# Kernel tuning notes

Hardware: AMD Instinct MI355X
Metric: run time of the kernel (lower is better)

## Reference

```python
import jax, jax.numpy as jnp
import numpy as np

N = 100000   # nodes
E = 1000000  # edges
DIN = 128    # atom_in_features
DE = 16      # edge_attr_dim
H = 128      # hidden width (preprocess/cheb/postprocess)
K = 3        # Chebyshev order
EPS = 1e-5


def setup_inputs() -> dict:
    key = jax.random.key(0)
    ks = jax.random.split(key, 16)
    s = 0.02
    return {
        "x": jax.random.normal(ks[0], (N, DIN), jnp.float32),
        "edge_index": jax.random.randint(ks[1], (2, E), 0, N),
        "edge_attr": jax.random.normal(ks[2], (E, DE), jnp.float32),
        # AtomEdgeInteraction linear: (DIN+DE) -> H
        "w_int": jax.random.normal(ks[3], (DIN + DE, H), jnp.float32) * s,
        "b_int": jnp.zeros((H,), jnp.float32),
        # preprocess layer 1: Linear + BatchNorm + ReLU
        "w_pre": jax.random.normal(ks[4], (H, H), jnp.float32) * s,
        "b_pre": jnp.zeros((H,), jnp.float32),
        "g_pre": jnp.ones((H,), jnp.float32),
        "be_pre": jnp.zeros((H,), jnp.float32),
        # ChebConv layers: weight [K, in, out] + bias
        "cheb1_w": jax.random.normal(ks[5], (K, H, H), jnp.float32) * s,
        "cheb1_b": jnp.zeros((H,), jnp.float32),
        "cheb2_w": jax.random.normal(ks[6], (K, H, H), jnp.float32) * s,
        "cheb2_b": jnp.zeros((H,), jnp.float32),
        # postprocess: Linear + BatchNorm + ReLU
        "w_post": jax.random.normal(ks[7], (H, H), jnp.float32) * s,
        "b_post": jnp.zeros((H,), jnp.float32),
        "g_post": jnp.ones((H,), jnp.float32),
        "be_post": jnp.zeros((H,), jnp.float32),
        # output layer H -> 1
        "w_out": jax.random.normal(ks[8], (H, 1), jnp.float32) * s,
        "b_out": jnp.zeros((1,), jnp.float32),
    }


def _bn(z, g, b):
    # BatchNorm1d, training-mode batch statistics (biased variance, like torch)
    m = z.mean(0)
    v = ((z - m) ** 2).mean(0)
    return g * (z - m) * jax.lax.rsqrt(v + EPS) + b


def _cheb(h, W, b, row, col, norm):
    # ChebConv with sym normalization, lambda_max=2 => L_hat = -D^{-1/2} A D^{-1/2}
    def lhat(z):
        return jax.ops.segment_sum(norm[:, None] * z[row], col, num_segments=N)

    Tx0 = h
    out = Tx0 @ W[0]
    Tx1 = lhat(Tx0)
    out = out + Tx1 @ W[1]
    for k in range(2, W.shape[0]):
        Tx2 = 2.0 * lhat(Tx1) - Tx0
        out = out + Tx2 @ W[k]
        Tx0, Tx1 = Tx1, Tx2
    return out + b


def reference(x, edge_index, edge_attr,
              w_int, b_int,
              w_pre, b_pre, g_pre, be_pre,
              cheb1_w, cheb1_b, cheb2_w, cheb2_b,
              w_post, b_post, g_post, be_post,
              w_out, b_out):
    row, col = edge_index[0], edge_index[1]
    ones_e = jnp.ones((E,), x.dtype)

    # AtomEdgeInteraction: gather -> concat -> linear -> scatter_mean over col
    comb = jnp.concatenate([x[row], edge_attr], axis=-1)  # [E, DIN+DE]
    upd = comb @ w_int + b_int                             # [E, H]
    cnt = jax.ops.segment_sum(ones_e, col, num_segments=N)
    h = jax.ops.segment_sum(upd, col, num_segments=N) / jnp.clip(cnt, 1.0)[:, None]

    # preprocess layer 1 (Linear + BN + ReLU; dropout rate 0)
    h = jax.nn.relu(_bn(h @ w_pre + b_pre, g_pre, be_pre))

    # sym-normalized edge coefficients for scaled Laplacian
    deg = jax.ops.segment_sum(ones_e, row, num_segments=N)
    dis = jnp.where(deg > 0, jax.lax.rsqrt(jnp.maximum(deg, 1.0)), 0.0)
    norm = -dis[row] * dis[col]  # [E]

    h = jax.nn.relu(_cheb(h, cheb1_w, cheb1_b, row, col, norm))
    h = jax.nn.relu(_cheb(h, cheb2_w, cheb2_b, row, col, norm))

    # postprocess (Linear + BN + ReLU)
    h = jax.nn.relu(_bn(h @ w_post + b_post, g_post, be_post))

    # output layer, squeeze(-1) -> [N]
    return (h @ w_out + b_out).squeeze(-1)
```

## Files before the change

### kernel.cpp

```cpp
#include <hip/hip_runtime.h>
#include <hip/hip_bf16.h>

using u16 = unsigned short;
using u32 = unsigned int;

#define NN 100000
#define NE 1000000

typedef __attribute__((ext_vector_type(8))) short bfrag;
typedef __attribute__((ext_vector_type(4))) float ffrag;

#define BF16ONE2 0x3F803F80u

__device__ __forceinline__ float bf2f(u16 u) { return __uint_as_float(((u32)u) << 16); }
__device__ __forceinline__ u16 f2bf(float f) {
  u32 x = __float_as_uint(f);
  return (u16)((x + 0x7fffu + ((x >> 16) & 1u)) >> 16);
}
__device__ __forceinline__ float rdv(const void* p, long i, int f) {
  return f ? bf2f(((const u16*)p)[i]) : ((const float*)p)[i];
}
__device__ __forceinline__ void acc8(float* a, uint4 v, float w) {
  a[0] = fmaf(w, __uint_as_float(v.x << 16), a[0]);
  a[1] = fmaf(w, __uint_as_float(v.x & 0xffff0000u), a[1]);
  a[2] = fmaf(w, __uint_as_float(v.y << 16), a[2]);
  a[3] = fmaf(w, __uint_as_float(v.y & 0xffff0000u), a[3]);
  a[4] = fmaf(w, __uint_as_float(v.z << 16), a[4]);
  a[5] = fmaf(w, __uint_as_float(v.z & 0xffff0000u), a[5]);
  a[6] = fmaf(w, __uint_as_float(v.w << 16), a[6]);
  a[7] = fmaf(w, __uint_as_float(v.w & 0xffff0000u), a[7]);
}

#define OWXT 0
#define OWPRE 16384
#define OWD1 32768
#define OW11 49152
#define OV21 65536
#define OWD2 81920
#define OW12 98304
#define OV22 114688
#define OWPOST 131072
#define OWET 147456

#define ASTRIDE 136
#define ESTRIDE 132

struct PrepArgs { const void* in[16]; };

__global__ void k_prep(PrepArgs a, const u32* __restrict__ gp, u16* __restrict__ wq,
                       float* __restrict__ wf) {
  int t = blockIdx.x * 256 + threadIdx.x;
  int f = (gp[0] == BF16ONE2) ? 1 : 0;
  if (t < 16384) {
    int o = t >> 7, k = t & 127;
    int ko = k * 128 + o;
    int ok = o * 128 + k;
    wq[OWXT + ok] = f2bf(rdv(a.in[0], ko, f));
    wq[OWPRE + ok] = f2bf(rdv(a.in[2], ko, f));
    float c0 = rdv(a.in[6], ko, f);
    float c1 = rdv(a.in[6], 16384 + ko, f);
    float c2 = rdv(a.in[6], 32768 + ko, f);
    wq[OWD1 + ok] = f2bf(c0 - c2);
    wq[OW11 + ok] = f2bf(c1);
    wq[OV21 + ok] = f2bf(2.f * c2);
    float d0 = rdv(a.in[8], ko, f);
    float d1 = rdv(a.in[8], 16384 + ko, f);
    float d2 = rdv(a.in[8], 32768 + ko, f);
    wq[OWD2 + ok] = f2bf(d0 - d2);
    wq[OW12 + ok] = f2bf(d1);
    wq[OV22 + ok] = f2bf(2.f * d2);
    wq[OWPOST + ok] = f2bf(rdv(a.in[10], ko, f));
  }
  if (t < 4096) {
    int o = t >> 5, k = t & 31;
    wq[OWET + o * 32 + k] = (k < 16) ? f2bf(rdv(a.in[0], (long)(128 + k) * 128 + o, f)) : (u16)0;
  }
  if (t < 1281) {
    int s = t >> 7, j = t & 127;
    const int map[11] = {1, 3, 4, 5, 7, 9, 11, 12, 13, 14, 15};
    wf[t] = rdv(a.in[map[s]], j, f);
  }
}

__global__ void k_hist(const int* __restrict__ ei, int* cnt) {
  long t = (long)blockIdx.x * 256 + threadIdx.x;
  long e0 = t * 8;
  if (e0 + 8 <= NE) {
    int4 c0 = *(const int4*)(ei + NE + e0);
    int4 c1 = *(const int4*)(ei + NE + e0 + 4);
    atomicAdd(&cnt[c0.x], 1);
    atomicAdd(&cnt[c0.y], 1);
    atomicAdd(&cnt[c0.z], 1);
    atomicAdd(&cnt[c0.w], 1);
    atomicAdd(&cnt[c1.x], 1);
    atomicAdd(&cnt[c1.y], 1);
    atomicAdd(&cnt[c1.z], 1);
    atomicAdd(&cnt[c1.w], 1);
  } else {
    for (long e = e0; e < NE; e++) atomicAdd(&cnt[ei[NE + e]], 1);
  }
}

__global__ void k_scan1(const int* __restrict__ cnt, int* off, int* bsum) {
  __shared__ int s[1024];
  int t = threadIdx.x;
  int g = blockIdx.x * 1024 + t;
  int v = (g < NN) ? cnt[g] : 0;
  s[t] = v;
  __syncthreads();
  for (int st = 1; st < 1024; st <<= 1) {
    int x = (t >= st) ? s[t - st] : 0;
    __syncthreads();
    s[t] += x;
    __syncthreads();
  }
  if (g < NN) off[g] = s[t] - v;
  if (t == 1023) bsum[blockIdx.x] = s[t];
}

__global__ void k_scan23(int* off, const int* __restrict__ bsum, int* cur, int nb) {
  __shared__ int s[128];
  int t = threadIdx.x;
  int v = 0;
  if (t < 128) {
    v = (t < nb) ? bsum[t] : 0;
    s[t] = v;
  }
  __syncthreads();
  for (int st = 1; st < 128; st <<= 1) {
    int x = (t >= st && t < 128) ? s[t - st] : 0;
    __syncthreads();
    if (t < 128) s[t] += x;
    __syncthreads();
  }
  if (t < 128) s[t] -= v;
  __syncthreads();
  int pre = s[blockIdx.x];
  int g = blockIdx.x * 1024 + t;
  if (g < NN) {
    int o = off[g] + pre;
    off[g] = o;
    cur[g] = o;
  }
  if (g == 0) off[NN] = NE;
}

__global__ void k_place(const int* __restrict__ ei, int* cur, int* deg,
                        int* __restrict__ crow, int* __restrict__ ceid) {
  long t = (long)blockIdx.x * 256 + threadIdx.x;
  long e0 = t * 8;
  if (e0 + 8 <= NE) {
    int4 r0 = *(const int4*)(ei + e0);
    int4 r1 = *(const int4*)(ei + e0 + 4);
    int4 c0 = *(const int4*)(ei + NE + e0);
    int4 c1 = *(const int4*)(ei + NE + e0 + 4);
    int r[8] = {r0.x, r0.y, r0.z, r0.w, r1.x, r1.y, r1.z, r1.w};
    int c[8] = {c0.x, c0.y, c0.z, c0.w, c1.x, c1.y, c1.z, c1.w};
    int p[8];
#pragma unroll
    for (int i = 0; i < 8; i++) p[i] = atomicAdd(&cur[c[i]], 1);
#pragma unroll
    for (int i = 0; i < 8; i++) atomicAdd(&deg[r[i]], 1);
#pragma unroll
    for (int i = 0; i < 8; i++) crow[p[i]] = r[i];
#pragma unroll
    for (int i = 0; i < 8; i++) ceid[p[i]] = (int)(e0 + i);
  } else {
    for (long e = e0; e < NE; e++) {
      int rr = ei[e], cc = ei[NE + e];
      int p = atomicAdd(&cur[cc], 1);
      atomicAdd(&deg[rr], 1);
      crow[p] = rr;
      ceid[p] = (int)e;
    }
  }
}

__global__ void k_dis(const int* __restrict__ deg, float* __restrict__ dis) {
  int g = blockIdx.x * 256 + threadIdx.x;
  if (g >= NN) return;
  int d = deg[g];
  dis[g] = d > 0 ? rsqrtf((float)d) : 0.f;
}

__global__ __launch_bounds__(256) void k_spmm(const u16* __restrict__ src,
                                              u16* __restrict__ dst,
                                              const int* __restrict__ off,
                                              const int* __restrict__ crow,
                                              const float* __restrict__ cnorm) {
  int t = threadIdx.x;
  int node = blockIdx.x * 8 + (t >> 5);
  if (node >= NN) return;
  int l = t & 31;
  int half = l >> 4;
  int c = (l & 15) * 8;
  int p0 = off[node], p1 = off[node + 1];
  float a[8];
#pragma unroll
  for (int j = 0; j < 8; j++) a[j] = 0.f;
  const u16* sp = src + c;
  int p = p0 + half;
  for (; p + 6 < p1; p += 8) {
    int r0 = crow[p], r1 = crow[p + 2], r2 = crow[p + 4], r3 = crow[p + 6];
    float w0 = cnorm[p], w1 = cnorm[p + 2], w2 = cnorm[p + 4], w3 = cnorm[p + 6];
    uint4 v0 = *(const uint4*)(sp + (long)r0 * 128);
    uint4 v1 = *(const uint4*)(sp + (long)r1 * 128);
    uint4 v2 = *(const uint4*)(sp + (long)r2 * 128);
    uint4 v3 = *(const uint4*)(sp + (long)r3 * 128);
    acc8(a, v0, w0);
    acc8(a, v1, w1);
    acc8(a, v2, w2);
    acc8(a, v3, w3);
  }
  for (; p < p1; p += 2) acc8(a, *(const uint4*)(sp + (long)crow[p] * 128), cnorm[p]);
#pragma unroll
  for (int j = 0; j < 8; j++) a[j] += __shfl_xor(a[j], 16);
  if (half) return;
  uint4 o;
  o.x = (u32)f2bf(a[0]) | ((u32)f2bf(a[1]) << 16);
  o.y = (u32)f2bf(a[2]) | ((u32)f2bf(a[3]) << 16);
  o.z = (u32)f2bf(a[4]) | ((u32)f2bf(a[5]) << 16);
  o.w = (u32)f2bf(a[6]) | ((u32)f2bf(a[7]) << 16);
  *(uint4*)(dst + (long)node * 128 + c) = o;
}

template <int WEIGHTED>
__device__ __forceinline__ void gather_lds(u16* sA, const u16* __restrict__ src,
                                           const int* __restrict__ off,
                                           const int* __restrict__ crow,
                                           const float* __restrict__ cnorm, int r0) {
  int tid = threadIdx.x;
  int grp = tid >> 4;
  int c = (tid & 15) * 8;
  const u16* sp = src + c;
#pragma unroll
  for (int i = 0; i < 4; i++) {
    int nl = grp * 4 + i;
    int node = r0 + nl;
    float a[8];
#pragma unroll
    for (int j = 0; j < 8; j++) a[j] = 0.f;
    if (node < NN) {
      int p0 = off[node], p1 = off[node + 1];
      int p = p0;
      for (; p + 4 <= p1; p += 4) {
        int r0i = crow[p], r1i = crow[p + 1], r2i = crow[p + 2], r3i = crow[p + 3];
        float w0 = WEIGHTED ? cnorm[p] : 1.f;
        float w1 = WEIGHTED ? cnorm[p + 1] : 1.f;
        float w2 = WEIGHTED ? cnorm[p + 2] : 1.f;
        float w3 = WEIGHTED ? cnorm[p + 3] : 1.f;
        uint4 v0 = *(const uint4*)(sp + (long)r0i * 128);
        uint4 v1 = *(const uint4*)(sp + (long)r1i * 128);
        uint4 v2 = *(const uint4*)(sp + (long)r2i * 128);
        uint4 v3 = *(const uint4*)(sp + (long)r3i * 128);
        acc8(a, v0, w0);
        acc8(a, v1, w1);
        acc8(a, v2, w2);
        acc8(a, v3, w3);
      }
      for (; p < p1; p++)
        acc8(a, *(const uint4*)(sp + (long)crow[p] * 128), WEIGHTED ? cnorm[p] : 1.f);
    }
    uint4 o;
    o.x = (u32)f2bf(a[0]) | ((u32)f2bf(a[1]) << 16);
    o.y = (u32)f2bf(a[2]) | ((u32)f2bf(a[3]) << 16);
    o.z = (u32)f2bf(a[4]) | ((u32)f2bf(a[5]) << 16);
    o.w = (u32)f2bf(a[6]) | ((u32)f2bf(a[7]) << 16);
    *(uint4*)(sA + nl * ASTRIDE + c) = o;
  }
}

__global__ __launch_bounds__(256) void k_asum(const void* __restrict__ eattr,
                                              const u32* __restrict__ gp,
                                              u16* __restrict__ asum,
                                              const int* __restrict__ off,
                                              const int* __restrict__ ceid,
                                              const int* __restrict__ crow,
                                              const float* __restrict__ dis,
                                              float* __restrict__ cnorm) {
  int t = blockIdx.x * 256 + threadIdx.x;
  int node = t >> 4;
  if (node >= NN) return;
  int j = t & 15;
  int p0 = off[node], p1 = off[node + 1];
  float ndis = -dis[node];
  for (int p = p0 + j; p < p1; p += 16) cnorm[p] = ndis * dis[crow[p]];
  float a = 0.f;
  if (gp[0] == BF16ONE2) {
    const u16* e16 = (const u16*)eattr;
    int p = p0;
    for (; p + 4 <= p1; p += 4) {
      float v0 = bf2f(e16[(long)ceid[p] * 16 + j]);
      float v1 = bf2f(e16[(long)ceid[p + 1] * 16 + j]);
      float v2 = bf2f(e16[(long)ceid[p + 2] * 16 + j]);
      float v3 = bf2f(e16[(long)ceid[p + 3] * 16 + j]);
      a += v0 + v1 + v2 + v3;
    }
    for (; p < p1; p++) a += bf2f(e16[(long)ceid[p] * 16 + j]);
  } else {
    const float* e32 = (const float*)eattr;
    int p = p0;
    for (; p + 4 <= p1; p += 4) {
      float v0 = e32[(long)ceid[p] * 16 + j];
      float v1 = e32[(long)ceid[p + 1] * 16 + j];
      float v2 = e32[(long)ceid[p + 2] * 16 + j];
      float v3 = e32[(long)ceid[p + 3] * 16 + j];
      a += v0 + v1 + v2 + v3;
    }
    for (; p < p1; p++) a += e32[(long)ceid[p] * 16 + j];
  }
  asum[(long)node * 16 + j] = f2bf(a);
}

struct MArgs {
  const void* A0; const u16* W0T; int a0raw;
  const float* bias;
  u16* out;
  const u32* gp;
  float* part;
};

__global__ __launch_bounds__(256) void k_mgemm(MArgs m) {
  constexpr int ROWS = 128, RT = 8, TPR = 2, SEGW = 64;
  __shared__ __align__(16) u16 sA[ROWS * ASTRIDE];
  int tid = threadIdx.x;
  int wv = tid >> 6, lane = tid & 63;
  int col16 = lane & 15, quad = lane >> 4;
  int r0 = blockIdx.x * ROWS;

  ffrag acc[RT * 2];
#pragma unroll
  for (int i = 0; i < RT * 2; i++)
#pragma unroll
    for (int g = 0; g < 4; g++) acc[i][g] = 0.f;

  {
    int row = tid / TPR, seg = tid % TPR;
    int ra = r0 + row;
    if (ra >= NN) ra = NN - 1;
    bool f32a = m.a0raw && (m.gp[0] != BF16ONE2);
    if (f32a) {
      const float* gs = (const float*)m.A0 + (long)ra * 128 + seg * SEGW;
      u32* lp = (u32*)(sA + row * ASTRIDE + seg * SEGW);
#pragma unroll
      for (int e = 0; e < SEGW / 8; e++) {
        float4 v0 = *(const float4*)(gs + e * 8);
        float4 v1 = *(const float4*)(gs + e * 8 + 4);
        lp[e * 4 + 0] = (u32)f2bf(v0.x) | ((u32)f2bf(v0.y) << 16);
        lp[e * 4 + 1] = (u32)f2bf(v0.z) | ((u32)f2bf(v0.w) << 16);
        lp[e * 4 + 2] = (u32)f2bf(v1.x) | ((u32)f2bf(v1.y) << 16);
        lp[e * 4 + 3] = (u32)f2bf(v1.z) | ((u32)f2bf(v1.w) << 16);
      }
    } else {
      const u16* gs = (const u16*)m.A0 + (long)ra * 128 + seg * SEGW;
      uint4* lp = (uint4*)(sA + row * ASTRIDE + seg * SEGW);
#pragma unroll
      for (int e = 0; e < SEGW / 8; e++) lp[e] = *(const uint4*)(gs + e * 8);
    }
  }
  bfrag b0[2][4];
#pragma unroll
  for (int c = 0; c < 2; c++)
#pragma unroll
    for (int kb = 0; kb < 4; kb++)
      b0[c][kb] = *(const bfrag*)(m.W0T + (long)(wv * 32 + c * 16 + col16) * 128 + kb * 32 + quad * 8);
  __syncthreads();
#pragma unroll
  for (int kb = 0; kb < 4; kb++)
#pragma unroll
    for (int rt = 0; rt < RT; rt++) {
      bfrag af = *(const bfrag*)(sA + (rt * 16 + col16) * ASTRIDE + kb * 32 + quad * 8);
      acc[rt * 2 + 0] = __builtin_amdgcn_mfma_f32_16x16x32_bf16(af, b0[0][kb], acc[rt * 2 + 0], 0, 0, 0);
      acc[rt * 2 + 1] = __builtin_amdgcn_mfma_f32_16x16x32_bf16(af, b0[1][kb], acc[rt * 2 + 1], 0, 0, 0);
    }
  __syncthreads();
#pragma unroll
  for (int rt = 0; rt < RT; rt++)
#pragma unroll
    for (int c = 0; c < 2; c++) {
      int col = wv * 32 + c * 16 + col16;
      float bj = m.bias ? m.bias[col] : 0.f;
#pragma unroll
      for (int g = 0; g < 4; g++)
        sA[(rt * 16 + quad * 4 + g) * ESTRIDE + col] = f2bf(acc[rt * 2 + c][g] + bj);
    }
  __syncthreads();
  {
    int rr = tid / TPR, d = tid % TPR;
    int rowg = r0 + rr;
    if (rowg < NN) {
      const u16* sp2 = sA + rr * ESTRIDE + d * 64;
      uint4* o = (uint4*)(m.out + (long)rowg * 128 + d * 64);
#pragma unroll
      for (int e = 0; e < 8; e++) {
        const uint2* s2 = (const uint2*)(sp2 + e * 8);
        uint2 lo = s2[0], hi = s2[1];
        o[e] = make_uint4(lo.x, lo.y, hi.x, hi.y);
      }
    }
  }
  if (m.part) {
    __shared__ float ps[256], pq[256];
    int col = tid & 127, hf = tid >> 7;
    float s = 0.f, q = 0.f;
#pragma unroll
    for (int r = 0; r < 64; r++) {
      int rr = hf * 64 + r;
      if (r0 + rr < NN) {
        float v = bf2f(sA[rr * ESTRIDE + col]);
        s += v;
        q += v * v;
      }
    }
    ps[tid] = s;
    pq[tid] = q;
    __syncthreads();
    if (tid < 128) {
      m.part[(long)blockIdx.x * 256 + tid] = ps[tid] + ps[tid + 128];
      m.part[(long)blockIdx.x * 256 + 128 + tid] = pq[tid] + pq[tid + 128];
    }
  }
}

__global__ __launch_bounds__(256) void k_etpre(const u16* __restrict__ Xg,
                                               const u16* __restrict__ asum,
                                               const u16* __restrict__ Wet,
                                               const u16* __restrict__ Wpre,
                                               const float* __restrict__ b_int,
                                               const float* __restrict__ b_pre,
                                               const int* __restrict__ off,
                                               const int* __restrict__ crow,
                                               u16* __restrict__ out, float* part) {
  __shared__ __align__(16) u16 sA[64 * ASTRIDE];
  int tid = threadIdx.x;
  int wv = tid >> 6, lane = tid & 63;
  int col16 = lane & 15, quad = lane >> 4;
  int r0 = blockIdx.x * 64;

  {
    int row = tid >> 2, seg = tid & 3;
    int ra = r0 + row;
    if (ra >= NN) ra = NN - 1;
    if (seg < 2)
      *(uint4*)(sA + row * ASTRIDE + seg * 8) = *(const uint4*)(asum + (long)ra * 16 + seg * 8);
    else
      *(uint4*)(sA + row * ASTRIDE + seg * 8) = make_uint4(0, 0, 0, 0);
  }
  bfrag be[2];
#pragma unroll
  for (int c = 0; c < 2; c++)
    be[c] = *(const bfrag*)(Wet + (long)(wv * 32 + c * 16 + col16) * 32 + quad * 8);
  __syncthreads();
  ffrag accE[8];
#pragma unroll
  for (int i = 0; i < 8; i++)
#pragma unroll
    for (int g = 0; g < 4; g++) accE[i][g] = 0.f;
#pragma unroll
  for (int rt = 0; rt < 4; rt++) {
    bfrag af = *(const bfrag*)(sA + (rt * 16 + col16) * ASTRIDE + quad * 8);
    accE[rt * 2 + 0] = __builtin_amdgcn_mfma_f32_16x16x32_bf16(af, be[0], accE[rt * 2 + 0], 0, 0, 0);
    accE[rt * 2 + 1] = __builtin_amdgcn_mfma_f32_16x16x32_bf16(af, be[1], accE[rt * 2 + 1], 0, 0, 0);
  }
  __syncthreads();
  gather_lds<0>(sA, Xg, off, crow, nullptr, r0);
  __syncthreads();
#pragma unroll
  for (int rt = 0; rt < 4; rt++)
#pragma unroll
    for (int g = 0; g < 4; g++) {
      int rr = rt * 16 + quad * 4 + g;
      int r = r0 + rr;
      int cc = (r < NN) ? off[r + 1] - off[r] : 0;
      float inv = 1.f / (float)(cc > 1 ? cc : 1);
#pragma unroll
      for (int c = 0; c < 2; c++) {
        int col = wv * 32 + c * 16 + col16;
        float bj = b_int[col];
        float v = accE[rt * 2 + c][g] + bf2f(sA[rr * ASTRIDE + col]);
        v = (v + (float)cc * bj) * inv;
        sA[rr * ASTRIDE + col] = f2bf(v);
      }
    }
  bfrag b1[2][4];
#pragma unroll
  for (int c = 0; c < 2; c++)
#pragma unroll
    for (int kb = 0; kb < 4; kb++)
      b1[c][kb] = *(const bfrag*)(Wpre + (long)(wv * 32 + c * 16 + col16) * 128 + kb * 32 + quad * 8);
  __syncthreads();
  ffrag a2[8];
#pragma unroll
  for (int i = 0; i < 8; i++)
#pragma unroll
    for (int g = 0; g < 4; g++) a2[i][g] = 0.f;
#pragma unroll
  for (int kb = 0; kb < 4; kb++)
#pragma unroll
    for (int rt = 0; rt < 4; rt++) {
      bfrag af = *(const bfrag*)(sA + (rt * 16 + col16) * ASTRIDE + kb * 32 + quad * 8);
      a2[rt * 2 + 0] = __builtin_amdgcn_mfma_f32_16x16x32_bf16(af, b1[0][kb], a2[rt * 2 + 0], 0, 0, 0);
      a2[rt * 2 + 1] = __builtin_amdgcn_mfma_f32_16x16x32_bf16(af, b1[1][kb], a2[rt * 2 + 1], 0, 0, 0);
    }
  __syncthreads();
#pragma unroll
  for (int rt = 0; rt < 4; rt++)
#pragma unroll
    for (int c = 0; c < 2; c++) {
      int col = wv * 32 + c * 16 + col16;
      float bj = b_pre[col];
#pragma unroll
      for (int g = 0; g < 4; g++)
        sA[(rt * 16 + quad * 4 + g) * ESTRIDE + col] = f2bf(a2[rt * 2 + c][g] + bj);
    }
  __syncthreads();
  {
    int rr = tid >> 2, d = tid & 3;
    int rowg = r0 + rr;
    if (rowg < NN) {
      const u16* sp2 = sA + rr * ESTRIDE + d * 32;
      uint4* o = (uint4*)(out + (long)rowg * 128 + d * 32);
#pragma unroll
      for (int e = 0; e < 4; e++) {
        const uint2* s2 = (const uint2*)(sp2 + e * 8);
        uint2 lo = s2[0], hi = s2[1];
        o[e] = make_uint4(lo.x, lo.y, hi.x, hi.y);
      }
    }
  }
  {
    __shared__ float ps[256], pq[256];
    int col = tid & 127, hf = tid >> 7;
    float s = 0.f, q = 0.f;
#pragma unroll
    for (int r = 0; r < 32; r++) {
      int rr = hf * 32 + r;
      if (r0 + rr < NN) {
        float v = bf2f(sA[rr * ESTRIDE + col]);
        s += v;
        q += v * v;
      }
    }
    ps[tid] = s;
    pq[tid] = q;
    __syncthreads();
    if (tid < 128) {
      part[(long)blockIdx.x * 256 + tid] = ps[tid] + ps[tid + 128];
      part[(long)blockIdx.x * 256 + 128 + tid] = pq[tid] + pq[tid + 128];
    }
  }
}

__global__ __launch_bounds__(256) void k_cheb(const u16* __restrict__ hb,
                                              const u16* __restrict__ T1,
                                              const int* __restrict__ off,
                                              const int* __restrict__ crow,
                                              const float* __restrict__ cnorm,
                                              const u16* __restrict__ WD,
                                              const u16* __restrict__ W1,
                                              const u16* __restrict__ V2,
                                              const float* __restrict__ bias,
                                              u16* __restrict__ out) {
  __shared__ __align__(16) u16 sA[64 * ASTRIDE];
  int tid = threadIdx.x;
  int wv = tid >> 6, lane = tid & 63;
  int col16 = lane & 15, quad = lane >> 4;
  int r0 = blockIdx.x * 64;

  ffrag acc[8];
#pragma unroll
  for (int i = 0; i < 8; i++)
#pragma unroll
    for (int g = 0; g < 4; g++) acc[i][g] = 0.f;

  gather_lds<1>(sA, T1, off, crow, cnorm, r0);
  bfrag bv[2][4];
#pragma unroll
  for (int c = 0; c < 2; c++)
#pragma unroll
    for (int kb = 0; kb < 4; kb++)
      bv[c][kb] = *(const bfrag*)(V2 + (long)(wv * 32 + c * 16 + col16) * 128 + kb * 32 + quad * 8);
  __syncthreads();
#pragma unroll
  for (int kb = 0; kb < 4; kb++)
#pragma unroll
    for (int rt = 0; rt < 4; rt++) {
      bfrag af = *(const bfrag*)(sA + (rt * 16 + col16) * ASTRIDE + kb * 32 + quad * 8);
      acc[rt * 2 + 0] = __builtin_amdgcn_mfma_f32_16x16x32_bf16(af, bv[0][kb], acc[rt * 2 + 0], 0, 0, 0);
      acc[rt * 2 + 1] = __builtin_amdgcn_mfma_f32_16x16x32_bf16(af, bv[1][kb], acc[rt * 2 + 1], 0, 0, 0);
    }
  __syncthreads();

  {
    int row = tid >> 2, seg = tid & 3;
    int ra = r0 + row;
    if (ra >= NN) ra = NN - 1;
    const u16* gs = hb + (long)ra * 128 + seg * 32;
    uint4* lp = (uint4*)(sA + row * ASTRIDE + seg * 32);
#pragma unroll
    for (int e = 0; e < 4; e++) lp[e] = *(const uint4*)(gs + e * 8);
  }
#pragma unroll
  for (int c = 0; c < 2; c++)
#pragma unroll
    for (int kb = 0; kb < 4; kb++)
      bv[c][kb] = *(const bfrag*)(WD + (long)(wv * 32 + c * 16 + col16) * 128 + kb * 32 + quad * 8);
  __syncthreads();
#pragma unroll
  for (int kb = 0; kb < 4; kb++)
#pragma unroll
    for (int rt = 0; rt < 4; rt++) {
      bfrag af = *(const bfrag*)(sA + (rt * 16 + col16) * ASTRIDE + kb * 32 + quad * 8);
      acc[rt * 2 + 0] = __builtin_amdgcn_mfma_f32_16x16x32_bf16(af, bv[0][kb], acc[rt * 2 + 0], 0, 0, 0);
      acc[rt * 2 + 1] = __builtin_amdgcn_mfma_f32_16x16x32_bf16(af, bv[1][kb], acc[rt * 2 + 1], 0, 0, 0);
    }
  __syncthreads();

  {
    int row = tid >> 2, seg = tid & 3;
    int ra = r0 + row;
    if (ra >= NN) ra = NN - 1;
    const u16* gs = T1 + (long)ra * 128 + seg * 32;
    uint4* lp = (uint4*)(sA + row * ASTRIDE + seg * 32);
#pragma unroll
    for (int e = 0; e < 4; e++) lp[e] = *(const uint4*)(gs + e * 8);
  }
#pragma unroll
  for (int c = 0; c < 2; c++)
#pragma unroll
    for (int kb = 0; kb < 4; kb++)
      bv[c][kb] = *(const bfrag*)(W1 + (long)(wv * 32 + c * 16 + col16) * 128 + kb * 32 + quad * 8);
  __syncthreads();
#pragma unroll
  for (int kb = 0; kb < 4; kb++)
#pragma unroll
    for (int rt = 0; rt < 4; rt++) {
      bfrag af = *(const bfrag*)(sA + (rt * 16 + col16) * ASTRIDE + kb * 32 + quad * 8);
      acc[rt * 2 + 0] = __builtin_amdgcn_mfma_f32_16x16x32_bf16(af, bv[0][kb], acc[rt * 2 + 0], 0, 0, 0);
      acc[rt * 2 + 1] = __builtin_amdgcn_mfma_f32_16x16x32_bf16(af, bv[1][kb], acc[rt * 2 + 1], 0, 0, 0);
    }
  __syncthreads();

#pragma unroll
  for (int rt = 0; rt < 4; rt++)
#pragma unroll
    for (int c = 0; c < 2; c++) {
      int col = wv * 32 + c * 16 + col16;
      float bj = bias[col];
#pragma unroll
      for (int g = 0; g < 4; g++)
        sA[(rt * 16 + quad * 4 + g) * ESTRIDE + col] = f2bf(fmaxf(acc[rt * 2 + c][g] + bj, 0.f));
    }
  __syncthreads();
  {
    int rr = tid >> 2, d = tid & 3;
    int rowg = r0 + rr;
    if (rowg < NN) {
      const u16* sp2 = sA + rr * ESTRIDE + d * 32;
      uint4* o = (uint4*)(out + (long)rowg * 128 + d * 32);
#pragma unroll
      for (int e = 0; e < 4; e++) {
        const uint2* s2 = (const uint2*)(sp2 + e * 8);
        uint2 lo = s2[0], hi = s2[1];
        o[e] = make_uint4(lo.x, lo.y, hi.x, hi.y);
      }
    }
  }
}

__global__ void k_redfin(const float* __restrict__ part, const float* __restrict__ gamma,
                         const float* __restrict__ beta, float* ab, int nblk) {
  int tid = threadIdx.x;
  int col = blockIdx.x * 16 + (tid & 15);
  int ch = tid >> 4;
  float s = 0.f, q = 0.f;
  for (int b = ch; b < nblk; b += 16) {
    s += part[(long)b * 256 + col];
    q += part[(long)b * 256 + 128 + col];
  }
  __shared__ float sh[256], qh[256];
  sh[tid] = s;
  qh[tid] = q;
  __syncthreads();
  if (tid < 16) {
    float ts = 0.f, tq = 0.f;
#pragma unroll
    for (int i = 0; i < 16; i++) {
      ts += sh[i * 16 + tid];
      tq += qh[i * 16 + tid];
    }
    int j = blockIdx.x * 16 + tid;
    float m = ts * (1.f / (float)NN);
    float v = fmaxf(tq * (1.f / (float)NN) - m * m, 0.f);
    float a = gamma[j] * rsqrtf(v + 1e-5f);
    ab[j] = a;
    ab[128 + j] = beta[j] - m * a;
  }
}

__global__ void k_bnrelu(const u16* __restrict__ z, u16* __restrict__ out,
                         const float* __restrict__ ab) {
  long idx = (long)blockIdx.x * 256 + threadIdx.x;
  long t = idx * 2;
  if (t >= (long)NN * 128) return;
  int col = (int)(t & 127);
  u32 v = *(const u32*)(z + t);
  float f0 = fmaxf(__uint_as_float(v << 16) * ab[col] + ab[128 + col], 0.f);
  float f1 = fmaxf(__uint_as_float(v & 0xffff0000u) * ab[col + 1] + ab[129 + col], 0.f);
  *(u32*)(out + t) = (u32)f2bf(f0) | ((u32)f2bf(f1) << 16);
}

__global__ void k_out(const u16* __restrict__ z, const float* __restrict__ ab,
                      const float* __restrict__ wout, const float* __restrict__ bout,
                      const u32* __restrict__ gp, void* __restrict__ y) {
  int node = blockIdx.x * 4 + (threadIdx.x >> 6);
  if (node >= NN) return;
  int lane = threadIdx.x & 63;
  float s = 0.f;
#pragma unroll
  for (int c = lane; c < 128; c += 64) {
    float zz = bf2f(z[(long)node * 128 + c]);
    float h = fmaxf(ab[c] * zz + ab[128 + c], 0.f);
    s += h * wout[c];
  }
#pragma unroll
  for (int o = 32; o > 0; o >>= 1) s += __shfl_down(s, o);
  if (lane == 0) {
    float r = s + bout[0];
    if (gp[0] == BF16ONE2) ((u16*)y)[node] = f2bf(r);
    else ((float*)y)[node] = r;
  }
}

extern "C" void kernel_launch(void* const* d_in, const int* in_sizes, int n_in,
                              void* d_out, int out_size, void* d_ws, size_t ws_size,
                              hipStream_t stream) {
  const void* x = d_in[0];
  const int* ei = (const int*)d_in[1];
  const void* eattr = d_in[2];
  const u32* gp = (const u32*)d_in[7];
  (void)in_sizes; (void)n_in; (void)out_size; (void)ws_size;

  char* w = (char*)d_ws;
  size_t p = 0;
  auto alloc = [&](size_t b) { size_t r = p; p += (b + 255) & ~(size_t)255; return r; };
  size_t o_cnt = alloc((size_t)NN * 4);
  size_t o_deg = alloc((size_t)NN * 4);
  size_t o_zero_end = p;
  size_t o_cur = alloc((size_t)NN * 4);
  size_t o_dis = alloc((size_t)NN * 4);
  size_t o_off = alloc((size_t)(NN + 1) * 4);
  size_t o_bsum = alloc(1024 * 4);
  size_t o_ab = alloc(512 * 4);
  size_t o_wq = alloc((size_t)151552 * 2);
  size_t o_wf = alloc((size_t)1281 * 4);
  size_t o_crow = alloc((size_t)NE * 4);
  size_t o_cnrm = alloc((size_t)NE * 4);
  size_t o_asum = alloc((size_t)NN * 16 * 2);
  size_t o_part = alloc((size_t)1563 * 256 * 4);
  size_t o_Bx = alloc((size_t)NN * 128 * 2);
  size_t o_Bt = alloc((size_t)NN * 128 * 2);

  int* cnt = (int*)(w + o_cnt);
  int* deg = (int*)(w + o_deg);
  int* cur = (int*)(w + o_cur);
  float* dis = (float*)(w + o_dis);
  int* off = (int*)(w + o_off);
  int* bsum = (int*)(w + o_bsum);
  float* abA = (float*)(w + o_ab);
  float* abB = abA + 256;
  u16* wq = (u16*)(w + o_wq);
  float* wf = (float*)(w + o_wf);
  int* crow = (int*)(w + o_crow);
  float* cnrm = (float*)(w + o_cnrm);
  u16* asum = (u16*)(w + o_asum);
  float* part = (float*)(w + o_part);
  u16* Bx = (u16*)(w + o_Bx);
  u16* Bt = (u16*)(w + o_Bt);
  int* ceid = (int*)Bt;

  hipMemsetAsync(w + o_cnt, 0, o_zero_end - o_cnt, stream);

  int gH = (NE / 8 + 255) / 256;
  int nb = (NN + 1023) / 1024;
  int gS = (NN + 7) / 8;
  int gN = (NN + 255) / 256;
  int gG1 = (NN + 127) / 128;
  int gG2 = (NN + 63) / 64;

  {
    PrepArgs a;
    for (int i = 0; i < 16; i++) a.in[i] = d_in[3 + i];
    k_prep<<<64, 256, 0, stream>>>(a, gp, wq, wf);
  }

  k_hist<<<gH, 256, 0, stream>>>(ei, cnt);
  k_scan1<<<nb, 1024, 0, stream>>>(cnt, off, bsum);
  k_scan23<<<nb, 1024, 0, stream>>>(off, bsum, cur, nb);
  k_place<<<gH, 256, 0, stream>>>(ei, cur, deg, crow, ceid);
  k_dis<<<gN, 256, 0, stream>>>(deg, dis);
  k_asum<<<(NN * 16 + 255) / 256, 256, 0, stream>>>(eattr, gp, asum, off, ceid, crow, dis, cnrm);

  {
    MArgs a = {};
    a.A0 = x; a.W0T = wq + OWXT; a.a0raw = 1;
    a.out = Bx; a.gp = gp;
    k_mgemm<<<gG1, 256, 0, stream>>>(a);
  }
  k_etpre<<<gG2, 256, 0, stream>>>(Bx, asum, wq + OWET, wq + OWPRE, wf + 0, wf + 128,
                                   off, crow, Bt, part);
  k_redfin<<<8, 256, 0, stream>>>(part, wf + 256, wf + 384, abA, gG2);
  k_bnrelu<<<(int)(((long)NN * 128 / 2 + 255) / 256), 256, 0, stream>>>(Bt, Bx, abA);

  k_spmm<<<gS, 256, 0, stream>>>(Bx, Bt, off, crow, cnrm);
  k_cheb<<<gG2, 256, 0, stream>>>(Bx, Bt, off, crow, cnrm,
                                  wq + OWD1, wq + OW11, wq + OV21, wf + 512, Bx);

  k_spmm<<<gS, 256, 0, stream>>>(Bx, Bt, off, crow, cnrm);
  k_cheb<<<gG2, 256, 0, stream>>>(Bx, Bt, off, crow, cnrm,
                                  wq + OWD2, wq + OW12, wq + OV22, wf + 640, Bx);

  {
    MArgs a = {};
    a.A0 = Bx; a.W0T = wq + OWPOST;
    a.bias = wf + 768; a.out = Bt; a.gp = gp; a.part = part;
    k_mgemm<<<gG1, 256, 0, stream>>>(a);
  }
  k_redfin<<<8, 256, 0, stream>>>(part, wf + 896, wf + 1024, abB, gG1);
  k_out<<<(NN + 3) / 4, 256, 0, stream>>>(Bt, abB, wf + 1152, wf + 1280, gp, d_out);
}
```

Before: 757.7 us.

## Fuse BN+ReLU into spmm and cheb, pack CSR row/edge ids, drop dis kernel

Removes the standalone BN+ReLU pass by applying the per-column affine and ReLU on the fly, both in the first spmm gather and when the first cheb kernel loads its dense rows. The separate crow and ceid arrays are merged into one int2 array. The degree normalisation is computed inside k_asum, so the k_dis kernel goes away. Gather loops become predicated fixed-width unrolls, and k_etpre gets a separate LDS buffer for edge sums so two barriers can be dropped. Packing row ids with edge ids doubles the bytes read per neighbour index in the spmm and cheb gathers, and activations are recomputed per neighbour instead of once.

```diff
diff --git a/kernel.cpp b/kernel.cpp
--- a/kernel.cpp
+++ b/kernel.cpp
@@ -29,6 +29,26 @@
   a[5] = fmaf(w, __uint_as_float(v.z & 0xffff0000u), a[5]);
   a[6] = fmaf(w, __uint_as_float(v.w << 16), a[6]);
   a[7] = fmaf(w, __uint_as_float(v.w & 0xffff0000u), a[7]);
+}
+__device__ __forceinline__ void acc8bn(float* a, uint4 v, float w, const float* A,
+                                       const float* Bb) {
+  float x;
+  x = __uint_as_float(v.x << 16);
+  a[0] = fmaf(w, fmaxf(fmaf(A[0], x, Bb[0]), 0.f), a[0]);
+  x = __uint_as_float(v.x & 0xffff0000u);
+  a[1] = fmaf(w, fmaxf(fmaf(A[1], x, Bb[1]), 0.f), a[1]);
+  x = __uint_as_float(v.y << 16);
+  a[2] = fmaf(w, fmaxf(fmaf(A[2], x, Bb[2]), 0.f), a[2]);
+  x = __uint_as_float(v.y & 0xffff0000u);
+  a[3] = fmaf(w, fmaxf(fmaf(A[3], x, Bb[3]), 0.f), a[3]);
+  x = __uint_as_float(v.z << 16);
+  a[4] = fmaf(w, fmaxf(fmaf(A[4], x, Bb[4]), 0.f), a[4]);
+  x = __uint_as_float(v.z & 0xffff0000u);
+  a[5] = fmaf(w, fmaxf(fmaf(A[5], x, Bb[5]), 0.f), a[5]);
+  x = __uint_as_float(v.w << 16);
+  a[6] = fmaf(w, fmaxf(fmaf(A[6], x, Bb[6]), 0.f), a[6]);
+  x = __uint_as_float(v.w & 0xffff0000u);
+  a[7] = fmaf(w, fmaxf(fmaf(A[7], x, Bb[7]), 0.f), a[7]);
 }
 
 #define OWXT 0
@@ -146,73 +166,77 @@
 }
 
 __global__ void k_place(const int* __restrict__ ei, int* cur, int* deg,
-                        int* __restrict__ crow, int* __restrict__ ceid) {
+                        int2* __restrict__ cpk) {
   long t = (long)blockIdx.x * 256 + threadIdx.x;
-  long e0 = t * 8;
-  if (e0 + 8 <= NE) {
-    int4 r0 = *(const int4*)(ei + e0);
-    int4 r1 = *(const int4*)(ei + e0 + 4);
-    int4 c0 = *(const int4*)(ei + NE + e0);
-    int4 c1 = *(const int4*)(ei + NE + e0 + 4);
-    int r[8] = {r0.x, r0.y, r0.z, r0.w, r1.x, r1.y, r1.z, r1.w};
-    int c[8] = {c0.x, c0.y, c0.z, c0.w, c1.x, c1.y, c1.z, c1.w};
-    int p[8];
-#pragma unroll
-    for (int i = 0; i < 8; i++) p[i] = atomicAdd(&cur[c[i]], 1);
-#pragma unroll
-    for (int i = 0; i < 8; i++) atomicAdd(&deg[r[i]], 1);
-#pragma unroll
-    for (int i = 0; i < 8; i++) crow[p[i]] = r[i];
-#pragma unroll
-    for (int i = 0; i < 8; i++) ceid[p[i]] = (int)(e0 + i);
+  long e0 = t * 4;
+  if (e0 + 4 <= NE) {
+    int4 r4 = *(const int4*)(ei + e0);
+    int4 c4 = *(const int4*)(ei + NE + e0);
+    int p0 = atomicAdd(&cur[c4.x], 1);
+    int p1 = atomicAdd(&cur[c4.y], 1);
+    int p2 = atomicAdd(&cur[c4.z], 1);
+    int p3 = atomicAdd(&cur[c4.w], 1);
+    atomicAdd(&deg[r4.x], 1);
+    atomicAdd(&deg[r4.y], 1);
+    atomicAdd(&deg[r4.z], 1);
+    atomicAdd(&deg[r4.w], 1);
+    cpk[p0] = make_int2(r4.x, (int)e0);
+    cpk[p1] = make_int2(r4.y, (int)e0 + 1);
+    cpk[p2] = make_int2(r4.z, (int)e0 + 2);
+    cpk[p3] = make_int2(r4.w, (int)e0 + 3);
   } else {
     for (long e = e0; e < NE; e++) {
       int rr = ei[e], cc = ei[NE + e];
       int p = atomicAdd(&cur[cc], 1);
       atomicAdd(&deg[rr], 1);
-      crow[p] = rr;
-      ceid[p] = (int)e;
-    }
-  }
-}
-
-__global__ void k_dis(const int* __restrict__ deg, float* __restrict__ dis) {
-  int g = blockIdx.x * 256 + threadIdx.x;
-  if (g >= NN) return;
-  int d = deg[g];
-  dis[g] = d > 0 ? rsqrtf((float)d) : 0.f;
-}
-
+      cpk[p] = make_int2(rr, (int)e);
+    }
+  }
+}
+
+template <int BN>
 __global__ __launch_bounds__(256) void k_spmm(const u16* __restrict__ src,
                                               u16* __restrict__ dst,
                                               const int* __restrict__ off,
-                                              const int* __restrict__ crow,
-                                              const float* __restrict__ cnorm) {
+                                              const int2* __restrict__ cpk,
+                                              const float* __restrict__ cnorm,
+                                              const float* __restrict__ ab) {
   int t = threadIdx.x;
   int node = blockIdx.x * 8 + (t >> 5);
   if (node >= NN) return;
   int l = t & 31;
   int half = l >> 4;
   int c = (l & 15) * 8;
+  float A[8], Bb[8];
+  if (BN) {
+#pragma unroll
+    for (int j = 0; j < 8; j++) {
+      A[j] = ab[c + j];
+      Bb[j] = ab[128 + c + j];
+    }
+  }
   int p0 = off[node], p1 = off[node + 1];
   float a[8];
 #pragma unroll
   for (int j = 0; j < 8; j++) a[j] = 0.f;
   const u16* sp = src + c;
-  int p = p0 + half;
-  for (; p + 6 < p1; p += 8) {
-    int r0 = crow[p], r1 = crow[p + 2], r2 = crow[p + 4], r3 = crow[p + 6];
-    float w0 = cnorm[p], w1 = cnorm[p + 2], w2 = cnorm[p + 4], w3 = cnorm[p + 6];
-    uint4 v0 = *(const uint4*)(sp + (long)r0 * 128);
-    uint4 v1 = *(const uint4*)(sp + (long)r1 * 128);
-    uint4 v2 = *(const uint4*)(sp + (long)r2 * 128);
-    uint4 v3 = *(const uint4*)(sp + (long)r3 * 128);
-    acc8(a, v0, w0);
-    acc8(a, v1, w1);
-    acc8(a, v2, w2);
-    acc8(a, v3, w3);
-  }
-  for (; p < p1; p += 2) acc8(a, *(const uint4*)(sp + (long)crow[p] * 128), cnorm[p]);
+  for (int p = p0 + half; p < p1; p += 8) {
+    int rr[4];
+    float w[4];
+#pragma unroll
+    for (int u = 0; u < 4; u++) {
+      int q = p + u * 2;
+      int qc = q < p1 ? q : p1 - 1;
+      rr[u] = cpk[qc].x;
+      w[u] = (q < p1) ? cnorm[qc] : 0.f;
+    }
+#pragma unroll
+    for (int u = 0; u < 4; u++) {
+      uint4 v = *(const uint4*)(sp + (long)rr[u] * 128);
+      if (BN) acc8bn(a, v, w[u], A, Bb);
+      else acc8(a, v, w[u]);
+    }
+  }
 #pragma unroll
   for (int j = 0; j < 8; j++) a[j] += __shfl_xor(a[j], 16);
   if (half) return;
@@ -227,7 +251,7 @@
 template <int WEIGHTED>
 __device__ __forceinline__ void gather_lds(u16* sA, const u16* __restrict__ src,
                                            const int* __restrict__ off,
-                                           const int* __restrict__ crow,
+                                           const int2* __restrict__ cpk,
                                            const float* __restrict__ cnorm, int r0) {
   int tid = threadIdx.x;
   int grp = tid >> 4;
@@ -242,24 +266,20 @@
     for (int j = 0; j < 8; j++) a[j] = 0.f;
     if (node < NN) {
       int p0 = off[node], p1 = off[node + 1];
-      int p = p0;
-      for (; p + 4 <= p1; p += 4) {
-        int r0i = crow[p], r1i = crow[p + 1], r2i = crow[p + 2], r3i = crow[p + 3];
-        float w0 = WEIGHTED ? cnorm[p] : 1.f;
-        float w1 = WEIGHTED ? cnorm[p + 1] : 1.f;
-        float w2 = WEIGHTED ? cnorm[p + 2] : 1.f;
-        float w3 = WEIGHTED ? cnorm[p + 3] : 1.f;
-        uint4 v0 = *(const uint4*)(sp + (long)r0i * 128);
-        uint4 v1 = *(const uint4*)(sp + (long)r1i * 128);
-        uint4 v2 = *(const uint4*)(sp + (long)r2i * 128);
-        uint4 v3 = *(const uint4*)(sp + (long)r3i * 128);
-        acc8(a, v0, w0);
-        acc8(a, v1, w1);
-        acc8(a, v2, w2);
-        acc8(a, v3, w3);
-      }
-      for (; p < p1; p++)
-        acc8(a, *(const uint4*)(sp + (long)crow[p] * 128), WEIGHTED ? cnorm[p] : 1.f);
+      for (int p = p0; p < p1; p += 8) {
+        int rr[8];
+        float w[8];
+#pragma unroll
+        for (int u = 0; u < 8; u++) {
+          int q = p + u;
+          int qc = q < p1 ? q : p1 - 1;
+          rr[u] = cpk[qc].x;
+          w[u] = (q < p1) ? (WEIGHTED ? cnorm[qc] : 1.f) : 0.f;
+        }
+#pragma unroll
+        for (int u = 0; u < 8; u++)
+          acc8(a, *(const uint4*)(sp + (long)rr[u] * 128), w[u]);
+      }
     }
     uint4 o;
     o.x = (u32)f2bf(a[0]) | ((u32)f2bf(a[1]) << 16);
@@ -274,40 +294,45 @@
                                               const u32* __restrict__ gp,
                                               u16* __restrict__ asum,
                                               const int* __restrict__ off,
-                                              const int* __restrict__ ceid,
-                                              const int* __restrict__ crow,
-                                              const float* __restrict__ dis,
+                                              const int2* __restrict__ cpk,
+                                              const int* __restrict__ deg,
                                               float* __restrict__ cnorm) {
   int t = blockIdx.x * 256 + threadIdx.x;
   int node = t >> 4;
   if (node >= NN) return;
   int j = t & 15;
   int p0 = off[node], p1 = off[node + 1];
-  float ndis = -dis[node];
-  for (int p = p0 + j; p < p1; p += 16) cnorm[p] = ndis * dis[crow[p]];
+  int dn = deg[node];
+  float ndis = dn > 0 ? -rsqrtf((float)dn) : 0.f;
+  for (int p = p0 + j; p < p1; p += 16)
+    cnorm[p] = ndis * rsqrtf((float)deg[cpk[p].x]);
   float a = 0.f;
   if (gp[0] == BF16ONE2) {
     const u16* e16 = (const u16*)eattr;
-    int p = p0;
-    for (; p + 4 <= p1; p += 4) {
-      float v0 = bf2f(e16[(long)ceid[p] * 16 + j]);
-      float v1 = bf2f(e16[(long)ceid[p + 1] * 16 + j]);
-      float v2 = bf2f(e16[(long)ceid[p + 2] * 16 + j]);
-      float v3 = bf2f(e16[(long)ceid[p + 3] * 16 + j]);
-      a += v0 + v1 + v2 + v3;
-    }
-    for (; p < p1; p++) a += bf2f(e16[(long)ceid[p] * 16 + j]);
+    for (int p = p0; p < p1; p += 8) {
+      float s[8];
+#pragma unroll
+      for (int u = 0; u < 8; u++) {
+        int q = p + u;
+        int qc = q < p1 ? q : p1 - 1;
+        float v = bf2f(e16[(long)cpk[qc].y * 16 + j]);
+        s[u] = (q < p1) ? v : 0.f;
+      }
+      a += ((s[0] + s[1]) + (s[2] + s[3])) + ((s[4] + s[5]) + (s[6] + s[7]));
+    }
   } else {
     const float* e32 = (const float*)eattr;
-    int p = p0;
-    for (; p + 4 <= p1; p += 4) {
-      float v0 = e32[(long)ceid[p] * 16 + j];
-      float v1 = e32[(long)ceid[p + 1] * 16 + j];
-      float v2 = e32[(long)ceid[p + 2] * 16 + j];
-      float v3 = e32[(long)ceid[p + 3] * 16 + j];
-      a += v0 + v1 + v2 + v3;
-    }
-    for (; p < p1; p++) a += e32[(long)ceid[p] * 16 + j];
+    for (int p = p0; p < p1; p += 8) {
+      float s[8];
+#pragma unroll
+      for (int u = 0; u < 8; u++) {
+        int q = p + u;
+        int qc = q < p1 ? q : p1 - 1;
+        float v = e32[(long)cpk[qc].y * 16 + j];
+        s[u] = (q < p1) ? v : 0.f;
+      }
+      a += ((s[0] + s[1]) + (s[2] + s[3])) + ((s[4] + s[5]) + (s[6] + s[7]));
+    }
   }
   asum[(long)node * 16 + j] = f2bf(a);
 }
@@ -429,22 +454,24 @@
                                                const float* __restrict__ b_int,
                                                const float* __restrict__ b_pre,
                                                const int* __restrict__ off,
-                                               const int* __restrict__ crow,
+                                               const int2* __restrict__ cpk,
                                                u16* __restrict__ out, float* part) {
   __shared__ __align__(16) u16 sA[64 * ASTRIDE];
+  __shared__ __align__(16) u16 sE[64 * 32];
   int tid = threadIdx.x;
   int wv = tid >> 6, lane = tid & 63;
   int col16 = lane & 15, quad = lane >> 4;
   int r0 = blockIdx.x * 64;
 
+  gather_lds<0>(sA, Xg, off, cpk, nullptr, r0);
   {
     int row = tid >> 2, seg = tid & 3;
     int ra = r0 + row;
     if (ra >= NN) ra = NN - 1;
     if (seg < 2)
-      *(uint4*)(sA + row * ASTRIDE + seg * 8) = *(const uint4*)(asum + (long)ra * 16 + seg * 8);
+      *(uint4*)(sE + row * 32 + seg * 8) = *(const uint4*)(asum + (long)ra * 16 + seg * 8);
     else
-      *(uint4*)(sA + row * ASTRIDE + seg * 8) = make_uint4(0, 0, 0, 0);
+      *(uint4*)(sE + row * 32 + seg * 8) = make_uint4(0, 0, 0, 0);
   }
   bfrag be[2];
 #pragma unroll
@@ -458,13 +485,10 @@
     for (int g = 0; g < 4; g++) accE[i][g] = 0.f;
 #pragma unroll
   for (int rt = 0; rt < 4; rt++) {
-    bfrag af = *(const bfrag*)(sA + (rt * 16 + col16) * ASTRIDE + quad * 8);
+    bfrag af = *(const bfrag*)(sE + (rt * 16 + col16) * 32 + quad * 8);
     accE[rt * 2 + 0] = __builtin_amdgcn_mfma_f32_16x16x32_bf16(af, be[0], accE[rt * 2 + 0], 0, 0, 0);
     accE[rt * 2 + 1] = __builtin_amdgcn_mfma_f32_16x16x32_bf16(af, be[1], accE[rt * 2 + 1], 0, 0, 0);
   }
-  __syncthreads();
-  gather_lds<0>(sA, Xg, off, crow, nullptr, r0);
-  __syncthreads();
 #pragma unroll
   for (int rt = 0; rt < 4; rt++)
 #pragma unroll
@@ -551,15 +575,17 @@
   }
 }
 
+template <int BN>
 __global__ __launch_bounds__(256) void k_cheb(const u16* __restrict__ hb,
                                               const u16* __restrict__ T1,
                                               const int* __restrict__ off,
-                                              const int* __restrict__ crow,
+                                              const int2* __restrict__ cpk,
                                               const float* __restrict__ cnorm,
                                               const u16* __restrict__ WD,
                                               const u16* __restrict__ W1,
                                               const u16* __restrict__ V2,
                                               const float* __restrict__ bias,
+                                              const float* __restrict__ ab,
                                               u16* __restrict__ out) {
   __shared__ __align__(16) u16 sA[64 * ASTRIDE];
   int tid = threadIdx.x;
@@ -567,13 +593,7 @@
   int col16 = lane & 15, quad = lane >> 4;
   int r0 = blockIdx.x * 64;
 
-  ffrag acc[8];
-#pragma unroll
-  for (int i = 0; i < 8; i++)
-#pragma unroll
-    for (int g = 0; g < 4; g++) acc[i][g] = 0.f;
-
-  gather_lds<1>(sA, T1, off, crow, cnorm, r0);
+  gather_lds<1>(sA, T1, off, cpk, cnorm, r0);
   bfrag bv[2][4];
 #pragma unroll
   for (int c = 0; c < 2; c++)
@@ -581,6 +601,11 @@
     for (int kb = 0; kb < 4; kb++)
       bv[c][kb] = *(const bfrag*)(V2 + (long)(wv * 32 + c * 16 + col16) * 128 + kb * 32 + quad * 8);
   __syncthreads();
+  ffrag acc[8];
+#pragma unroll
+  for (int i = 0; i < 8; i++)
+#pragma unroll
+    for (int g = 0; g < 4; g++) acc[i][g] = 0.f;
 #pragma unroll
   for (int kb = 0; kb < 4; kb++)
 #pragma unroll
@@ -597,8 +622,30 @@
     if (ra >= NN) ra = NN - 1;
     const u16* gs = hb + (long)ra * 128 + seg * 32;
     uint4* lp = (uint4*)(sA + row * ASTRIDE + seg * 32);
-#pragma unroll
-    for (int e = 0; e < 4; e++) lp[e] = *(const uint4*)(gs + e * 8);
+    if (BN) {
+#pragma unroll
+      for (int e = 0; e < 4; e++) {
+        uint4 v = *(const uint4*)(gs + e * 8);
+        int cb = seg * 32 + e * 8;
+        float f0 = fmaxf(fmaf(ab[cb + 0], __uint_as_float(v.x << 16), ab[128 + cb + 0]), 0.f);
+        float f1 = fmaxf(fmaf(ab[cb + 1], __uint_as_float(v.x & 0xffff0000u), ab[128 + cb + 1]), 0.f);
+        float f2 = fmaxf(fmaf(ab[cb + 2], __uint_as_float(v.y << 16), ab[128 + cb + 2]), 0.f);
+        float f3 = fmaxf(fmaf(ab[cb + 3], __uint_as_float(v.y & 0xffff0000u), ab[128 + cb + 3]), 0.f);
+        float f4 = fmaxf(fmaf(ab[cb + 4], __uint_as_float(v.z << 16), ab[128 + cb + 4]), 0.f);
+        float f5 = fmaxf(fmaf(ab[cb + 5], __uint_as_float(v.z & 0xffff0000u), ab[128 + cb + 5]), 0.f);
+        float f6 = fmaxf(fmaf(ab[cb + 6], __uint_as_float(v.w << 16), ab[128 + cb + 6]), 0.f);
+        float f7 = fmaxf(fmaf(ab[cb + 7], __uint_as_float(v.w & 0xffff0000u), ab[128 + cb + 7]), 0.f);
+        uint4 o;
+        o.x = (u32)f2bf(f0) | ((u32)f2bf(f1) << 16);
+        o.y = (u32)f2bf(f2) | ((u32)f2bf(f3) << 16);
+        o.z = (u32)f2bf(f4) | ((u32)f2bf(f5) << 16);
+        o.w = (u32)f2bf(f6) | ((u32)f2bf(f7) << 16);
+        lp[e] = o;
+      }
+    } else {
+#pragma unroll
+      for (int e = 0; e < 4; e++) lp[e] = *(const uint4*)(gs + e * 8);
+    }
   }
 #pragma unroll
   for (int c = 0; c < 2; c++)
@@ -698,18 +745,6 @@
   }
 }
 
-__global__ void k_bnrelu(const u16* __restrict__ z, u16* __restrict__ out,
-                         const float* __restrict__ ab) {
-  long idx = (long)blockIdx.x * 256 + threadIdx.x;
-  long t = idx * 2;
-  if (t >= (long)NN * 128) return;
-  int col = (int)(t & 127);
-  u32 v = *(const u32*)(z + t);
-  float f0 = fmaxf(__uint_as_float(v << 16) * ab[col] + ab[128 + col], 0.f);
-  float f1 = fmaxf(__uint_as_float(v & 0xffff0000u) * ab[col + 1] + ab[129 + col], 0.f);
-  *(u32*)(out + t) = (u32)f2bf(f0) | ((u32)f2bf(f1) << 16);
-}
-
 __global__ void k_out(const u16* __restrict__ z, const float* __restrict__ ab,
                       const float* __restrict__ wout, const float* __restrict__ bout,
                       const u32* __restrict__ gp, void* __restrict__ y) {
@@ -748,13 +783,12 @@
   size_t o_deg = alloc((size_t)NN * 4);
   size_t o_zero_end = p;
   size_t o_cur = alloc((size_t)NN * 4);
-  size_t o_dis = alloc((size_t)NN * 4);
   size_t o_off = alloc((size_t)(NN + 1) * 4);
   size_t o_bsum = alloc(1024 * 4);
   size_t o_ab = alloc(512 * 4);
   size_t o_wq = alloc((size_t)151552 * 2);
   size_t o_wf = alloc((size_t)1281 * 4);
-  size_t o_crow = alloc((size_t)NE * 4);
+  size_t o_cpk = alloc((size_t)NE * 8);
   size_t o_cnrm = alloc((size_t)NE * 4);
   size_t o_asum = alloc((size_t)NN * 16 * 2);
   size_t o_part = alloc((size_t)1563 * 256 * 4);
@@ -764,27 +798,25 @@
   int* cnt = (int*)(w + o_cnt);
   int* deg = (int*)(w + o_deg);
   int* cur = (int*)(w + o_cur);
-  float* dis = (float*)(w + o_dis);
   int* off = (int*)(w + o_off);
   int* bsum = (int*)(w + o_bsum);
   float* abA = (float*)(w + o_ab);
   float* abB = abA + 256;
   u16* wq = (u16*)(w + o_wq);
   float* wf = (float*)(w + o_wf);
-  int* crow = (int*)(w + o_crow);
+  int2* cpk = (int2*)(w + o_cpk);
   float* cnrm = (float*)(w + o_cnrm);
   u16* asum = (u16*)(w + o_asum);
   float* part = (float*)(w + o_part);
   u16* Bx = (u16*)(w + o_Bx);
   u16* Bt = (u16*)(w + o_Bt);
-  int* ceid = (int*)Bt;
 
   hipMemsetAsync(w + o_cnt, 0, o_zero_end - o_cnt, stream);
 
   int gH = (NE / 8 + 255) / 256;
+  int gP = (NE / 4 + 255) / 256;
   int nb = (NN + 1023) / 1024;
   int gS = (NN + 7) / 8;
-  int gN = (NN + 255) / 256;
   int gG1 = (NN + 127) / 128;
   int gG2 = (NN + 63) / 64;
 
@@ -797,9 +829,8 @@
   k_hist<<<gH, 256, 0, stream>>>(ei, cnt);
   k_scan1<<<nb, 1024, 0, stream>>>(cnt, off, bsum);
   k_scan23<<<nb, 1024, 0, stream>>>(off, bsum, cur, nb);
-  k_place<<<gH, 256, 0, stream>>>(ei, cur, deg, crow, ceid);
-  k_dis<<<gN, 256, 0, stream>>>(deg, dis);
-  k_asum<<<(NN * 16 + 255) / 256, 256, 0, stream>>>(eattr, gp, asum, off, ceid, crow, dis, cnrm);
+  k_place<<<gP, 256, 0, stream>>>(ei, cur, deg, cpk);
+  k_asum<<<(NN * 16 + 255) / 256, 256, 0, stream>>>(eattr, gp, asum, off, cpk, deg, cnrm);
 
   {
     MArgs a = {};
@@ -808,24 +839,23 @@
     k_mgemm<<<gG1, 256, 0, stream>>>(a);
   }
   k_etpre<<<gG2, 256, 0, stream>>>(Bx, asum, wq + OWET, wq + OWPRE, wf + 0, wf + 128,
-                                   off, crow, Bt, part);
+                                   off, cpk, Bt, part);
   k_redfin<<<8, 256, 0, stream>>>(part, wf + 256, wf + 384, abA, gG2);
-  k_bnrelu<<<(int)(((long)NN * 128 / 2 + 255) / 256), 256, 0, stream>>>(Bt, Bx, abA);
-
-  k_spmm<<<gS, 256, 0, stream>>>(Bx, Bt, off, crow, cnrm);
-  k_cheb<<<gG2, 256, 0, stream>>>(Bx, Bt, off, crow, cnrm,
-                                  wq + OWD1, wq + OW11, wq + OV21, wf + 512, Bx);
-
-  k_spmm<<<gS, 256, 0, stream>>>(Bx, Bt, off, crow, cnrm);
-  k_cheb<<<gG2, 256, 0, stream>>>(Bx, Bt, off, crow, cnrm,
-                                  wq + OWD2, wq + OW12, wq + OV22, wf + 640, Bx);
+
+  k_spmm<1><<<gS, 256, 0, stream>>>(Bt, Bx, off, cpk, cnrm, abA);
+  k_cheb<1><<<gG2, 256, 0, stream>>>(Bt, Bx, off, cpk, cnrm,
+                                     wq + OWD1, wq + OW11, wq + OV21, wf + 512, abA, Bt);
+
+  k_spmm<0><<<gS, 256, 0, stream>>>(Bt, Bx, off, cpk, cnrm, nullptr);
+  k_cheb<0><<<gG2, 256, 0, stream>>>(Bt, Bx, off, cpk, cnrm,
+                                     wq + OWD2, wq + OW12, wq + OV22, wf + 640, nullptr, Bt);
 
   {
     MArgs a = {};
-    a.A0 = Bx; a.W0T = wq + OWPOST;
-    a.bias = wf + 768; a.out = Bt; a.gp = gp; a.part = part;
+    a.A0 = Bt; a.W0T = wq + OWPOST;
+    a.bias = wf + 768; a.out = Bx; a.gp = gp; a.part = part;
     k_mgemm<<<gG1, 256, 0, stream>>>(a);
   }
   k_redfin<<<8, 256, 0, stream>>>(part, wf + 896, wf + 1024, abB, gG1);
-  k_out<<<(NN + 3) / 4, 256, 0, stream>>>(Bt, abB, wf + 1152, wf + 1280, gp, d_out);
-}
+  k_out<<<(NN + 3) / 4, 256, 0, stream>>>(Bx, abB, wf + 1152, wf + 1280, gp, d_out);
+}
```

Result: faster. 739.4 us (-2.4%).
